# Kernel optimization log

Hardware: AMD Instinct MI355X
Metric: run time of the kernel (lower is better)

Reference implementation:

```python
import jax, jax.numpy as jnp
import numpy as np

B = 32; IMG = 224; P = 16; D = 768; NH = 12; HD = 64; L = 12; MLP = 3072; S0 = 197
NE = 10; LP = 40; NPL = 5; NC = 100; EPS = 1e-6
POS_PROMPT = (0, 1, 2, 3, 4)


def setup_inputs() -> dict:
    ks = jax.random.split(jax.random.key(0), 18)
    n = lambda k, shp: jax.random.normal(k, shp, jnp.float32) * 0.02
    return {
        "inputs": jax.random.normal(ks[0], (B, 3, IMG, IMG), jnp.float32),
        "expert_ids": jax.random.randint(ks[1], (B,), 0, NE),
        "patch_w": n(ks[2], (D, 3, P, P)),
        "patch_b": n(ks[3], (D,)),
        "cls_token": n(ks[4], (1, 1, D)),
        "pos_embed": n(ks[5], (1, S0, D)),
        "ln1_s": jnp.ones((L, D), jnp.float32),
        "ln1_b": jnp.zeros((L, D), jnp.float32),
        "qkv_w": n(ks[6], (L, D, 3 * D)),
        "qkv_b": n(ks[7], (L, 3 * D)),
        "proj_w": n(ks[8], (L, D, D)),
        "proj_b": n(ks[9], (L, D)),
        "ln2_s": jnp.ones((L, D), jnp.float32),
        "ln2_b": jnp.zeros((L, D), jnp.float32),
        "fc1_w": n(ks[10], (L, D, MLP)),
        "fc1_b": n(ks[11], (L, MLP)),
        "fc2_w": n(ks[12], (L, MLP, D)),
        "fc2_b": n(ks[13], (L, D)),
        "norm_s": jnp.ones((D,), jnp.float32),
        "norm_b": jnp.zeros((D,), jnp.float32),
        "prompts": jax.random.uniform(ks[14], (NPL, NE, LP, D), jnp.float32),
        "head_w": n(ks[15], (NE, D, NC)),
        "head_b": n(ks[16], (NE, NC)),
    }


def _ln(x, s, b):
    m = x.mean(-1, keepdims=True)
    v = ((x - m) ** 2).mean(-1, keepdims=True)
    return (x - m) * jax.lax.rsqrt(v + EPS) * s + b


def _forward(inputs, expert_ids, patch_w, patch_b, cls_token, pos_embed,
             ln1_s, ln1_b, qkv_w, qkv_b, proj_w, proj_b, ln2_s, ln2_b,
             fc1_w, fc1_b, fc2_w, fc2_b, norm_s, norm_b, prompts, head_w, head_b):
    # patch embed: conv stride 16 -> [B, D, 14, 14] -> [B, 196, D]
    x = jax.lax.conv_general_dilated(inputs, patch_w, (P, P), 'VALID',
                                     dimension_numbers=('NCHW', 'OIHW', 'NCHW'))
    x = x.reshape(B, D, -1).transpose(0, 2, 1) + patch_b
    x = jnp.concatenate([jnp.broadcast_to(cls_token, (B, 1, D)), x], axis=1) + pos_embed
    # per-sample expert prompt gather: [B, NPL, LP, D], plus cls pos bias
    bp = jnp.take(prompts, expert_ids, axis=1).transpose(1, 0, 2, 3) + pos_embed[0, 0]
    scale = 1.0 / np.sqrt(HD)
    for i in range(L):
        if i in POS_PROMPT:
            x = jnp.concatenate([x, bp[:, POS_PROMPT.index(i)]], axis=1)
        S = x.shape[1]
        h = _ln(x, ln1_s[i], ln1_b[i])
        qkv = (h @ qkv_w[i] + qkv_b[i]).reshape(B, S, 3, NH, HD).transpose(2, 0, 3, 1, 4)
        q, k, v = qkv[0], qkv[1], qkv[2]
        att = jax.nn.softmax(jnp.einsum('bhqd,bhkd->bhqk', q, k) * scale, axis=-1)
        o = jnp.einsum('bhqk,bhkd->bhqd', att, v).transpose(0, 2, 1, 3).reshape(B, S, D)
        x = x + o @ proj_w[i] + proj_b[i]
        h = _ln(x, ln2_s[i], ln2_b[i])
        x = x + jax.nn.gelu(h @ fc1_w[i] + fc1_b[i], approximate=False) @ fc2_w[i] + fc2_b[i]
        x = x[:, :S0]  # drop prompt tokens after each block
    feat = _ln(x, norm_s, norm_b)[:, 0]
    # per-sample expert head dispatch: gathered-weight batched matvec
    return jnp.einsum('bd,bdc->bc', feat, head_w[expert_ids]) + head_b[expert_ids]


def reference(inputs, expert_ids, patch_w, patch_b, cls_token, pos_embed,
              ln1_s, ln1_b, qkv_w, qkv_b, proj_w, proj_b, ln2_s, ln2_b,
              fc1_w, fc1_b, fc2_w, fc2_b, norm_s, norm_b, prompts, head_w, head_b):
    return _forward(inputs, expert_ids, patch_w, patch_b, cls_token, pos_embed,
                    ln1_s, ln1_b, qkv_w, qkv_b, proj_w, proj_b, ln2_s, ln2_b,
                    fc1_w, fc1_b, fc2_w, fc2_b, norm_s, norm_b, prompts, head_w, head_b)
```

## Files before the change

kernel.cpp:

```cpp
#include <hip/hip_runtime.h>

typedef unsigned short ushort_t;
typedef __attribute__((ext_vector_type(8))) short short8;
typedef __attribute__((ext_vector_type(4))) float floatx4;

#define D_    768
#define SMAX  237
#define S0_   197
#define RPAD  7680
#define NHEAD 12
#define BATCH 32


__device__ __forceinline__ ushort_t f2bf(float f) {
  union { float f; unsigned u; } v; v.f = f;
  unsigned r = v.u + 0x7FFFu + ((v.u >> 16) & 1u);
  return (ushort_t)(r >> 16);
}
__device__ __forceinline__ float bf2f(ushort_t u) {
  union { unsigned u; float f; } v; v.u = ((unsigned)u) << 16; return v.f;
}
__device__ __forceinline__ void async16(const void* g, void* l) {
  __builtin_amdgcn_global_load_lds((const __attribute__((address_space(1))) void*)g,
                                   (__attribute__((address_space(3))) void*)l, 16, 0, 0);
}

__global__ __launch_bounds__(256) void patchify_kernel(
    const float* __restrict__ in, ushort_t* __restrict__ Xp) {
  int rowid = blockIdx.x;
  int b = rowid / 196, p = rowid - b * 196;
  int py = p / 14, px = p - py * 14;
  int tid = threadIdx.x;
#pragma unroll
  for (int t = 0; t < 3; ++t) {
    int k = tid + t * 256;
    int c = k >> 8, rem = k & 255, i = rem >> 4, j = rem & 15;
    float v = in[(((size_t)b * 3 + c) * 224 + py * 16 + i) * 224 + px * 16 + j];
    Xp[(size_t)rowid * 768 + k] = f2bf(v);
  }
}

__global__ void cvt_bf16_kernel(const float* __restrict__ src, ushort_t* __restrict__ dst, int n) {
  int i = blockIdx.x * 256 + threadIdx.x;
  if (i < n) dst[i] = f2bf(src[i]);
}

__global__ void cls_fill_kernel(const float* __restrict__ cls, const float* __restrict__ pos,
                                float* __restrict__ X) {
  int b = blockIdx.x, d = threadIdx.x;
  X[(size_t)b * 768 + d] = cls[d] + pos[d];
}

__global__ void prompt_fill_kernel(const float* __restrict__ prompts, const float* __restrict__ pos,
                                   const int* __restrict__ eid, float* __restrict__ X, int layer) {
  int id = blockIdx.x;
  int b = id / 40, p = id - b * 40;
  int e = eid[b];
  float v = prompts[(((size_t)layer * 10 + e) * 40 + p) * 768 + threadIdx.x] + pos[threadIdx.x];
  X[((size_t)(197 + p) * 32 + b) * 768 + threadIdx.x] = v;
}

__global__ __launch_bounds__(256) void transpose_wts_kernel(
    const float* __restrict__ qkvw, const float* __restrict__ projw,
    const float* __restrict__ fc1w, const float* __restrict__ fc2w,
    ushort_t* __restrict__ wq, ushort_t* __restrict__ wp,
    ushort_t* __restrict__ w1, ushort_t* __restrict__ w2,
    int l0, int slot_mul) {
  int id = blockIdx.x;
  int l = l0 + id / 6912;
  int t = id % 6912;
  size_t s = (size_t)(l * slot_mul);
  const float* src; ushort_t* dst; int K, N;
  if (t < 1728)      { src = qkvw + (size_t)l * 768 * 2304; dst = wq + s * 2304 * 768; K = 768;  N = 2304; }
  else if (t < 2304) { src = projw + (size_t)l * 768 * 768;  dst = wp + s * 768 * 768;  K = 768;  N = 768;  t -= 1728; }
  else if (t < 4608) { src = fc1w + (size_t)l * 768 * 3072;  dst = w1 + s * 768 * 3072; K = 768;  N = 3072; t -= 2304; }
  else               { src = fc2w + (size_t)l * 3072 * 768;  dst = w2 + s * 3072 * 768; K = 3072; N = 768;  t -= 4608; }
  int ntn = N >> 5;
  int k0 = (t / ntn) * 32, n0 = (t % ntn) * 32;
  __shared__ float tile[32][33];
  int tx = threadIdx.x & 31, ty = threadIdx.x >> 5;
#pragma unroll
  for (int q = 0; q < 4; ++q) {
    int kk = q * 8 + ty;
    tile[kk][tx] = src[(size_t)(k0 + kk) * N + n0 + tx];
  }
  __syncthreads();
#pragma unroll
  for (int q = 0; q < 4; ++q) {
    int nn = q * 8 + ty;
    dst[(size_t)(n0 + nn) * K + k0 + tx] = f2bf(tile[tx][nn]);
  }
}

__global__ __launch_bounds__(256) void ln_kernel(
    const float* __restrict__ X, const float* __restrict__ s, const float* __restrict__ bt,
    ushort_t* __restrict__ H) {
  int row = blockIdx.x, tid = threadIdx.x;
  const float* xr = X + (size_t)row * 768;
  float v0 = xr[tid], v1 = xr[tid + 256], v2 = xr[tid + 512];
  float sum = v0 + v1 + v2;
  float sq = v0 * v0 + v1 * v1 + v2 * v2;
#pragma unroll
  for (int off = 32; off; off >>= 1) {
    sum += __shfl_down(sum, off, 64);
    sq  += __shfl_down(sq,  off, 64);
  }
  __shared__ float red[8];
  int wv = tid >> 6, ln = tid & 63;
  if (ln == 0) { red[wv] = sum; red[4 + wv] = sq; }
  __syncthreads();
  if (tid == 0) {
    red[0] = red[0] + red[1] + red[2] + red[3];
    red[4] = red[4] + red[5] + red[6] + red[7];
  }
  __syncthreads();
  float mean = red[0] * (1.f / 768.f);
  float var  = red[4] * (1.f / 768.f) - mean * mean;
  float rs = rsqrtf(var + 1e-6f);
  ushort_t* hr = H + (size_t)row * 768;
  hr[tid]       = f2bf((v0 - mean) * rs * s[tid]       + bt[tid]);
  hr[tid + 256] = f2bf((v1 - mean) * rs * s[tid + 256] + bt[tid + 256]);
  hr[tid + 512] = f2bf((v2 - mean) * rs * s[tid + 512] + bt[tid + 512]);
}

enum { EPI_BF16 = 0, EPI_GELU = 1, EPI_RESID = 2, EPI_PATCH = 3 };

template <int EPI>
__device__ __forceinline__ void epi_store(float accv, int row, int col,
                                          const float* bias, float* XO, ushort_t* O,
                                          const float* pos, int N) {
  if (EPI == EPI_BF16) {
    O[(size_t)row * N + col] = f2bf(accv + bias[col]);
  } else if (EPI == EPI_GELU) {
    float v = accv + bias[col];
    float g = 0.5f * v * (1.0f + erff(v * 0.70710678118f));
    O[(size_t)row * N + col] = f2bf(g);
  } else if (EPI == EPI_RESID) {
    XO[(size_t)row * 768 + col] += accv + bias[col];
  } else {
    int b = row / 196, p = row - b * 196;
    size_t orow = (size_t)(1 + p) * 32 + b;
    XO[orow * 768 + col] = accv + bias[col] + pos[(size_t)(1 + p) * 768 + col];
  }
}

template <int EPI>
__global__ __launch_bounds__(256) void gemm_kernel(
    const ushort_t* __restrict__ A, int lda,
    const ushort_t* __restrict__ BT,
    const float* __restrict__ bias,
    float* __restrict__ XO, ushort_t* __restrict__ O,
    const float* __restrict__ pos,
    int N, int K) {
  __shared__ ushort_t As[128 * 32];
  __shared__ ushort_t Bs[128 * 32];
  int m0 = blockIdx.y * 128, n0 = blockIdx.x * 128;
  int tid = threadIdx.x, lane = tid & 63, wv = tid >> 6;
  int wm = (wv >> 1) * 64, wn = (wv & 1) * 64;
  int fr = lane & 15, kg = lane >> 4;
  int sw = (kg ^ ((fr >> 1) & 3)) * 8;

  floatx4 acc[4][4];
#pragma unroll
  for (int i = 0; i < 4; ++i)
#pragma unroll
    for (int j = 0; j < 4; ++j) acc[i][j] = (floatx4){0.f, 0.f, 0.f, 0.f};

  for (int k0 = 0; k0 < K; k0 += 32) {
#pragma unroll
    for (int t = 0; t < 2; ++t) {
      int flat = (wv * 2 + t) * 64 + lane;
      int row = flat >> 2;
      int ch = ((flat & 3) ^ ((flat >> 3) & 3)) * 8;
      async16(A + (size_t)(m0 + row) * lda + k0 + ch, &As[(wv * 2 + t) * 512]);
      async16(BT + (size_t)(n0 + row) * K + k0 + ch, &Bs[(wv * 2 + t) * 512]);
    }
    __syncthreads();
    short8 af[4], bfr[4];
#pragma unroll
    for (int i = 0; i < 4; ++i) af[i] = *(const short8*)&As[(wm + i * 16 + fr) * 32 + sw];
#pragma unroll
    for (int j = 0; j < 4; ++j) bfr[j] = *(const short8*)&Bs[(wn + j * 16 + fr) * 32 + sw];
#pragma unroll
    for (int i = 0; i < 4; ++i)
#pragma unroll
      for (int j = 0; j < 4; ++j)
        acc[i][j] = __builtin_amdgcn_mfma_f32_16x16x32_bf16(af[i], bfr[j], acc[i][j], 0, 0, 0);
    __syncthreads();
  }

  int rbase = (lane >> 4) * 4;
#pragma unroll
  for (int i = 0; i < 4; ++i)
#pragma unroll
    for (int j = 0; j < 4; ++j) {
      int col = n0 + wn + j * 16 + fr;
#pragma unroll
      for (int r = 0; r < 4; ++r)
        epi_store<EPI>(acc[i][j][r], m0 + wm + i * 16 + rbase + r, col, bias, XO, O, pos, N);
    }
}

template <int EPI>
__global__ __launch_bounds__(256) void gemm64_kernel(
    const ushort_t* __restrict__ A, int lda,
    const ushort_t* __restrict__ BT,
    const float* __restrict__ bias,
    float* __restrict__ XO, ushort_t* __restrict__ O,
    const float* __restrict__ pos,
    int N, int K) {
  __shared__ ushort_t As[64 * 32];
  __shared__ ushort_t Bs[128 * 32];
  int m0 = blockIdx.y * 64, n0 = blockIdx.x * 128;
  int tid = threadIdx.x, lane = tid & 63, wv = tid >> 6;
  int wm = (wv >> 1) * 32, wn = (wv & 1) * 64;
  int fr = lane & 15, kg = lane >> 4;
  int sw = (kg ^ ((fr >> 1) & 3)) * 8;

  floatx4 acc[2][4];
#pragma unroll
  for (int i = 0; i < 2; ++i)
#pragma unroll
    for (int j = 0; j < 4; ++j) acc[i][j] = (floatx4){0.f, 0.f, 0.f, 0.f};

  for (int k0 = 0; k0 < K; k0 += 32) {
    {
      int flat = wv * 64 + lane;
      int row = flat >> 2;
      int ch = ((flat & 3) ^ ((flat >> 3) & 3)) * 8;
      async16(A + (size_t)(m0 + row) * lda + k0 + ch, &As[wv * 512]);
    }
#pragma unroll
    for (int t = 0; t < 2; ++t) {
      int flat = (wv * 2 + t) * 64 + lane;
      int row = flat >> 2;
      int ch = ((flat & 3) ^ ((flat >> 3) & 3)) * 8;
      async16(BT + (size_t)(n0 + row) * K + k0 + ch, &Bs[(wv * 2 + t) * 512]);
    }
    __syncthreads();
    short8 af[2], bfr[4];
#pragma unroll
    for (int i = 0; i < 2; ++i) af[i] = *(const short8*)&As[(wm + i * 16 + fr) * 32 + sw];
#pragma unroll
    for (int j = 0; j < 4; ++j) bfr[j] = *(const short8*)&Bs[(wn + j * 16 + fr) * 32 + sw];
#pragma unroll
    for (int i = 0; i < 2; ++i)
#pragma unroll
      for (int j = 0; j < 4; ++j)
        acc[i][j] = __builtin_amdgcn_mfma_f32_16x16x32_bf16(af[i], bfr[j], acc[i][j], 0, 0, 0);
    __syncthreads();
  }

  int rbase = (lane >> 4) * 4;
#pragma unroll
  for (int i = 0; i < 2; ++i)
#pragma unroll
    for (int j = 0; j < 4; ++j) {
      int col = n0 + wn + j * 16 + fr;
#pragma unroll
      for (int r = 0; r < 4; ++r)
        epi_store<EPI>(acc[i][j][r], m0 + wm + i * 16 + rbase + r, col, bias, XO, O, pos, N);
    }
}

__global__ __launch_bounds__(256) void attn_kernel(ushort_t* __restrict__ qkv, int S) {
  __shared__ ushort_t Kc[64 * 64];
  __shared__ ushort_t Vt[64 * 72];
  __shared__ ushort_t Pb[4][16 * 72];
  int id = blockIdx.x;
  int qc = id & 3, bh = id >> 2;
  int b = bh / NHEAD, h = bh - b * NHEAD;
  int tid = threadIdx.x, lane = tid & 63, wv = tid >> 6;
  int fr = lane & 15, kg = lane >> 4;
  int q0 = qc * 64 + wv * 16;

  int qr = q0 + fr; if (qr > S - 1) qr = S - 1;
  const ushort_t* qp = qkv + ((size_t)qr * 32 + b) * 2304 + h * 64 + kg * 8;
  short8 qf0 = *(const short8*)qp;
  short8 qf1 = *(const short8*)(qp + 32);

  floatx4 oacc[4];
#pragma unroll
  for (int j = 0; j < 4; ++j) oacc[j] = (floatx4){0.f, 0.f, 0.f, 0.f};
  float lsum[4] = {0.f, 0.f, 0.f, 0.f};

  int ksw = kg ^ (fr & 7);
  int kst_g = (lane & 7) ^ ((lane >> 3) & 7);

  for (int c = 0; c < 4; ++c) {
    int key0 = c * 64;
    __syncthreads();
#pragma unroll
    for (int t = 0; t < 2; ++t) {
      int f = (wv * 2 + t) * 64 + lane;
      int kr = key0 + (f >> 3); if (kr > S - 1) kr = S - 1;
      async16(qkv + ((size_t)kr * 32 + b) * 2304 + 768 + h * 64 + kst_g * 8,
              &Kc[(wv * 2 + t) * 512]);
    }
#pragma unroll
    for (int t = 0; t < 2; ++t) {
      int kc = wv * 2 + t;
      int vr = key0 + lane; if (vr > S - 1) vr = S - 1;
      short8 vv = *(const short8*)(qkv + ((size_t)vr * 32 + b) * 2304 + 1536 + h * 64 + kc * 8);
#pragma unroll
      for (int e = 0; e < 8; ++e) Vt[(kc * 8 + e) * 72 + lane] = (ushort_t)vv[e];
    }
    __syncthreads();

    floatx4 sacc[4];
#pragma unroll
    for (int j = 0; j < 4; ++j) sacc[j] = (floatx4){0.f, 0.f, 0.f, 0.f};
#pragma unroll
    for (int j = 0; j < 4; ++j) {
      int krow = j * 16 + fr;
      short8 b0 = *(const short8*)&Kc[krow * 64 + ksw * 8];
      short8 b1 = *(const short8*)&Kc[krow * 64 + (ksw ^ 4) * 8];
      sacc[j] = __builtin_amdgcn_mfma_f32_16x16x32_bf16(qf0, b0, sacc[j], 0, 0, 0);
      sacc[j] = __builtin_amdgcn_mfma_f32_16x16x32_bf16(qf1, b1, sacc[j], 0, 0, 0);
    }

#pragma unroll
    for (int j = 0; j < 4; ++j) {
      int key = key0 + j * 16 + fr;
      bool valid = key < S;
#pragma unroll
      for (int r = 0; r < 4; ++r) {
        float e = valid ? __expf(sacc[j][r] * 0.125f) : 0.f;
        lsum[r] += e;
        Pb[wv][(kg * 4 + r) * 72 + j * 16 + fr] = f2bf(e);
      }
    }
    __syncthreads();

    const ushort_t* pp = &Pb[wv][fr * 72 + kg * 8];
    short8 p0 = *(const short8*)pp;
    short8 p1 = *(const short8*)(pp + 32);
#pragma unroll
    for (int j = 0; j < 4; ++j) {
      const ushort_t* vp = &Vt[(j * 16 + fr) * 72 + kg * 8];
      short8 v0 = *(const short8*)vp;
      short8 v1 = *(const short8*)(vp + 32);
      oacc[j] = __builtin_amdgcn_mfma_f32_16x16x32_bf16(p0, v0, oacc[j], 0, 0, 0);
      oacc[j] = __builtin_amdgcn_mfma_f32_16x16x32_bf16(p1, v1, oacc[j], 0, 0, 0);
    }
  }

#pragma unroll
  for (int r = 0; r < 4; ++r) {
#pragma unroll
    for (int m = 1; m <= 8; m <<= 1) lsum[r] += __shfl_xor(lsum[r], m, 64);
  }
#pragma unroll
  for (int r = 0; r < 4; ++r) {
    int q = q0 + kg * 4 + r;
    if (q < S) {
      float inv = 1.f / lsum[r];
      ushort_t* op = qkv + ((size_t)q * 32 + b) * 2304 + h * 64;
#pragma unroll
      for (int j = 0; j < 4; ++j) op[j * 16 + fr] = f2bf(oacc[j][r] * inv);
    }
  }
}

__global__ __launch_bounds__(256) void head_kernel(
    const float* __restrict__ X, const float* __restrict__ ns, const float* __restrict__ nb,
    const int* __restrict__ eid, const float* __restrict__ hw, const float* __restrict__ hb,
    float* __restrict__ out) {
  int b = blockIdx.x, tid = threadIdx.x;
  const float* xr = X + (size_t)b * 768;
  float v0 = xr[tid], v1 = xr[tid + 256], v2 = xr[tid + 512];
  float sum = v0 + v1 + v2;
  float sq = v0 * v0 + v1 * v1 + v2 * v2;
#pragma unroll
  for (int off = 32; off; off >>= 1) {
    sum += __shfl_down(sum, off, 64);
    sq  += __shfl_down(sq,  off, 64);
  }
  __shared__ float red[8];
  __shared__ float feat[768];
  int wv = tid >> 6, ln = tid & 63;
  if (ln == 0) { red[wv] = sum; red[4 + wv] = sq; }
  __syncthreads();
  if (tid == 0) {
    red[0] = red[0] + red[1] + red[2] + red[3];
    red[4] = red[4] + red[5] + red[6] + red[7];
  }
  __syncthreads();
  float mean = red[0] * (1.f / 768.f);
  float var  = red[4] * (1.f / 768.f) - mean * mean;
  float rs = rsqrtf(var + 1e-6f);
  feat[tid]       = (v0 - mean) * rs * ns[tid]       + nb[tid];
  feat[tid + 256] = (v1 - mean) * rs * ns[tid + 256] + nb[tid + 256];
  feat[tid + 512] = (v2 - mean) * rs * ns[tid + 512] + nb[tid + 512];
  __syncthreads();
  int e = eid[b];
  if (tid < 100) {
    float a = hb[e * 100 + tid];
    const float* w = hw + (size_t)e * 768 * 100 + tid;
#pragma unroll 4
    for (int d = 0; d < 768; ++d) a += feat[d] * w[(size_t)d * 100];
    out[b * 100 + tid] = a;
  }
}

extern "C" void kernel_launch(void* const* d_in, const int* in_sizes, int n_in,
                              void* d_out, int out_size, void* d_ws, size_t ws_size,
                              hipStream_t stream) {
  const float* inputs     = (const float*)d_in[0];
  const int*   expert_ids = (const int*)d_in[1];
  const float* patch_w    = (const float*)d_in[2];
  const float* patch_b    = (const float*)d_in[3];
  const float* cls_token  = (const float*)d_in[4];
  const float* pos_embed  = (const float*)d_in[5];
  const float* ln1_s      = (const float*)d_in[6];
  const float* ln1_b      = (const float*)d_in[7];
  const float* qkv_w      = (const float*)d_in[8];
  const float* qkv_b      = (const float*)d_in[9];
  const float* proj_w     = (const float*)d_in[10];
  const float* proj_b     = (const float*)d_in[11];
  const float* ln2_s      = (const float*)d_in[12];
  const float* ln2_b      = (const float*)d_in[13];
  const float* fc1_w      = (const float*)d_in[14];
  const float* fc1_b      = (const float*)d_in[15];
  const float* fc2_w      = (const float*)d_in[16];
  const float* fc2_b      = (const float*)d_in[17];
  const float* norm_s     = (const float*)d_in[18];
  const float* norm_b     = (const float*)d_in[19];
  const float* prompts    = (const float*)d_in[20];
  const float* head_w     = (const float*)d_in[21];
  const float* head_b     = (const float*)d_in[22];
  float* out = (float*)d_out;

  const size_t kHoistNeed = 289100000ull;
  bool hoist = ws_size >= kHoistNeed;
  size_t slots = hoist ? 12 : 1;

  char* ws = (char*)d_ws;
  size_t off = 0;
  ushort_t* WTp = (ushort_t*)(ws + off); off += (size_t)768 * 768 * 2;
  ushort_t* WQ  = (ushort_t*)(ws + off); off += slots * 2304 * 768 * 2;
  ushort_t* WP  = (ushort_t*)(ws + off); off += slots * 768 * 768 * 2;
  ushort_t* W1  = (ushort_t*)(ws + off); off += slots * 768 * 3072 * 2;
  ushort_t* W2  = (ushort_t*)(ws + off); off += slots * 3072 * 768 * 2;
  float*    X   = (float*)(ws + off);    off += (size_t)RPAD * 768 * 4;
  ushort_t* H   = (ushort_t*)(ws + off); off += (size_t)RPAD * 768 * 2;
  ushort_t* QKV = (ushort_t*)(ws + off); off += (size_t)RPAD * 2304 * 2;
  ushort_t* MID = (ushort_t*)(ws + off); off += (size_t)RPAD * 3072 * 2;
  ushort_t* XP  = MID;

  cvt_bf16_kernel<<<(768 * 768 + 255) / 256, 256, 0, stream>>>(patch_w, WTp, 768 * 768);
  patchify_kernel<<<6272, 256, 0, stream>>>(inputs, XP);
  gemm64_kernel<EPI_PATCH><<<dim3(6, 98), 256, 0, stream>>>(
      XP, 768, WTp, patch_b, X, nullptr, pos_embed, 768, 768);
  cls_fill_kernel<<<BATCH, 768, 0, stream>>>(cls_token, pos_embed, X);

  if (hoist)
    transpose_wts_kernel<<<6912 * 12, 256, 0, stream>>>(
        qkv_w, proj_w, fc1_w, fc2_w, WQ, WP, W1, W2, 0, 1);

  for (int i = 0; i < 12; ++i) {
    int S = (i < 5) ? SMAX : S0_;
    int MT = (i < 5) ? 60 : 50;
    if (i < 5)
      prompt_fill_kernel<<<BATCH * 40, 768, 0, stream>>>(prompts, pos_embed, expert_ids, X, i);
    if (!hoist)
      transpose_wts_kernel<<<6912, 256, 0, stream>>>(
          qkv_w, proj_w, fc1_w, fc2_w, WQ, WP, W1, W2, i, 0);
    ushort_t* WQi = WQ + (hoist ? (size_t)i * 2304 * 768 : 0);
    ushort_t* WPi = WP + (hoist ? (size_t)i * 768 * 768 : 0);
    ushort_t* W1i = W1 + (hoist ? (size_t)i * 768 * 3072 : 0);
    ushort_t* W2i = W2 + (hoist ? (size_t)i * 3072 * 768 : 0);

    ln_kernel<<<MT * 128, 256, 0, stream>>>(X, ln1_s + i * 768, ln1_b + i * 768, H);
    gemm_kernel<EPI_BF16><<<dim3(18, MT), 256, 0, stream>>>(
        H, 768, WQi, qkv_b + i * 2304, nullptr, QKV, nullptr, 2304, 768);
    attn_kernel<<<BATCH * NHEAD * 4, 256, 0, stream>>>(QKV, S);
    gemm64_kernel<EPI_RESID><<<dim3(6, MT * 2), 256, 0, stream>>>(
        QKV, 2304, WPi, proj_b + i * 768, X, nullptr, nullptr, 768, 768);
    ln_kernel<<<MT * 128, 256, 0, stream>>>(X, ln2_s + i * 768, ln2_b + i * 768, H);
    gemm_kernel<EPI_GELU><<<dim3(24, MT), 256, 0, stream>>>(
        H, 768, W1i, fc1_b + i * 3072, nullptr, MID, nullptr, 3072, 768);
    gemm64_kernel<EPI_RESID><<<dim3(6, MT * 2), 256, 0, stream>>>(
        MID, 3072, W2i, fc2_b + i * 768, X, nullptr, nullptr, 768, 3072);
  }

  head_kernel<<<BATCH, 256, 0, stream>>>(X, norm_s, norm_b, expert_ids, head_w, head_b, out);
}
```

Before: 3.508 ms.

## Deepen GEMM K-tile to 64, vectorize LN and weight transpose, retile residual GEMMs

The GEMM kernels now stage 64-wide K slices in LDS with an 8-way XOR swizzle and run two MFMA sub-steps per barrier pair, halving the number of synchronisations per K. Layernorm processes one row per wavefront with vector loads and shuffle-only reductions, which removes the shared-memory barriers. The weight transpose uses 64x64 tiles with vector loads and 16-byte bf16 stores. The proj and fc2 residual GEMMs switch from 64-row to 128-row tiles, trading fewer blocks for more reuse.

```diff
diff --git a/kernel.cpp b/kernel.cpp
--- a/kernel.cpp
+++ b/kernel.cpp
@@ -2,6 +2,7 @@
 
 typedef unsigned short ushort_t;
 typedef __attribute__((ext_vector_type(8))) short short8;
+typedef __attribute__((ext_vector_type(4))) short shortx4;
 typedef __attribute__((ext_vector_type(4))) float floatx4;
 
 #define D_    768
@@ -67,60 +68,72 @@
     ushort_t* __restrict__ w1, ushort_t* __restrict__ w2,
     int l0, int slot_mul) {
   int id = blockIdx.x;
-  int l = l0 + id / 6912;
-  int t = id % 6912;
+  int l = l0 + id / 1728;
+  int t = id % 1728;
   size_t s = (size_t)(l * slot_mul);
   const float* src; ushort_t* dst; int K, N;
-  if (t < 1728)      { src = qkvw + (size_t)l * 768 * 2304; dst = wq + s * 2304 * 768; K = 768;  N = 2304; }
-  else if (t < 2304) { src = projw + (size_t)l * 768 * 768;  dst = wp + s * 768 * 768;  K = 768;  N = 768;  t -= 1728; }
-  else if (t < 4608) { src = fc1w + (size_t)l * 768 * 3072;  dst = w1 + s * 768 * 3072; K = 768;  N = 3072; t -= 2304; }
-  else               { src = fc2w + (size_t)l * 3072 * 768;  dst = w2 + s * 3072 * 768; K = 3072; N = 768;  t -= 4608; }
-  int ntn = N >> 5;
-  int k0 = (t / ntn) * 32, n0 = (t % ntn) * 32;
-  __shared__ float tile[32][33];
-  int tx = threadIdx.x & 31, ty = threadIdx.x >> 5;
+  if (t < 432)       { src = qkvw + (size_t)l * 768 * 2304; dst = wq + s * 2304 * 768; K = 768;  N = 2304; }
+  else if (t < 576)  { src = projw + (size_t)l * 768 * 768;  dst = wp + s * 768 * 768;  K = 768;  N = 768;  t -= 432; }
+  else if (t < 1152) { src = fc1w + (size_t)l * 768 * 3072;  dst = w1 + s * 768 * 3072; K = 768;  N = 3072; t -= 576; }
+  else               { src = fc2w + (size_t)l * 3072 * 768;  dst = w2 + s * 3072 * 768; K = 3072; N = 768;  t -= 1152; }
+  int ntn = N >> 6;
+  int k0 = (t / ntn) * 64, n0 = (t % ntn) * 64;
+  __shared__ float tile[64][65];
+  int tid = threadIdx.x;
 #pragma unroll
   for (int q = 0; q < 4; ++q) {
-    int kk = q * 8 + ty;
-    tile[kk][tx] = src[(size_t)(k0 + kk) * N + n0 + tx];
+    int slot = q * 256 + tid;
+    int r = slot >> 4, c4 = (slot & 15) * 4;
+    floatx4 v = *(const floatx4*)&src[(size_t)(k0 + r) * N + n0 + c4];
+    tile[r][c4] = v[0]; tile[r][c4 + 1] = v[1]; tile[r][c4 + 2] = v[2]; tile[r][c4 + 3] = v[3];
   }
   __syncthreads();
 #pragma unroll
-  for (int q = 0; q < 4; ++q) {
-    int nn = q * 8 + ty;
-    dst[(size_t)(n0 + nn) * K + k0 + tx] = f2bf(tile[tx][nn]);
+  for (int q = 0; q < 2; ++q) {
+    int slot = q * 256 + tid;
+    int n = slot >> 3, kc = (slot & 7) * 8;
+    short8 o;
+#pragma unroll
+    for (int e = 0; e < 8; ++e) o[e] = (short)f2bf(tile[kc + e][n]);
+    *(short8*)&dst[(size_t)(n0 + n) * K + k0 + kc] = o;
   }
 }
 
 __global__ __launch_bounds__(256) void ln_kernel(
     const float* __restrict__ X, const float* __restrict__ s, const float* __restrict__ bt,
     ushort_t* __restrict__ H) {
-  int row = blockIdx.x, tid = threadIdx.x;
+  int row = blockIdx.x * 4 + (threadIdx.x >> 6);
+  int lane = threadIdx.x & 63;
   const float* xr = X + (size_t)row * 768;
-  float v0 = xr[tid], v1 = xr[tid + 256], v2 = xr[tid + 512];
-  float sum = v0 + v1 + v2;
-  float sq = v0 * v0 + v1 * v1 + v2 * v2;
-#pragma unroll
-  for (int off = 32; off; off >>= 1) {
-    sum += __shfl_down(sum, off, 64);
-    sq  += __shfl_down(sq,  off, 64);
-  }
-  __shared__ float red[8];
-  int wv = tid >> 6, ln = tid & 63;
-  if (ln == 0) { red[wv] = sum; red[4 + wv] = sq; }
-  __syncthreads();
-  if (tid == 0) {
-    red[0] = red[0] + red[1] + red[2] + red[3];
-    red[4] = red[4] + red[5] + red[6] + red[7];
-  }
-  __syncthreads();
-  float mean = red[0] * (1.f / 768.f);
-  float var  = red[4] * (1.f / 768.f) - mean * mean;
+  floatx4 v0 = *(const floatx4*)&xr[lane * 4];
+  floatx4 v1 = *(const floatx4*)&xr[256 + lane * 4];
+  floatx4 v2 = *(const floatx4*)&xr[512 + lane * 4];
+  float sum = 0.f, sq = 0.f;
+#pragma unroll
+  for (int e = 0; e < 4; ++e) {
+    sum += v0[e] + v1[e] + v2[e];
+    sq  += v0[e] * v0[e] + v1[e] * v1[e] + v2[e] * v2[e];
+  }
+#pragma unroll
+  for (int m = 1; m <= 32; m <<= 1) {
+    sum += __shfl_xor(sum, m, 64);
+    sq  += __shfl_xor(sq,  m, 64);
+  }
+  float mean = sum * (1.f / 768.f);
+  float var  = sq * (1.f / 768.f) - mean * mean;
   float rs = rsqrtf(var + 1e-6f);
   ushort_t* hr = H + (size_t)row * 768;
-  hr[tid]       = f2bf((v0 - mean) * rs * s[tid]       + bt[tid]);
-  hr[tid + 256] = f2bf((v1 - mean) * rs * s[tid + 256] + bt[tid + 256]);
-  hr[tid + 512] = f2bf((v2 - mean) * rs * s[tid + 512] + bt[tid + 512]);
+#pragma unroll
+  for (int w = 0; w < 3; ++w) {
+    const floatx4 v = (w == 0) ? v0 : (w == 1) ? v1 : v2;
+    shortx4 o;
+#pragma unroll
+    for (int e = 0; e < 4; ++e) {
+      int d = w * 256 + lane * 4 + e;
+      o[e] = (short)f2bf((v[e] - mean) * rs * s[d] + bt[d]);
+    }
+    *(shortx4*)&hr[w * 256 + lane * 4] = o;
+  }
 }
 
 enum { EPI_BF16 = 0, EPI_GELU = 1, EPI_RESID = 2, EPI_PATCH = 3 };
@@ -152,13 +165,13 @@
     float* __restrict__ XO, ushort_t* __restrict__ O,
     const float* __restrict__ pos,
     int N, int K) {
-  __shared__ ushort_t As[128 * 32];
-  __shared__ ushort_t Bs[128 * 32];
+  __shared__ ushort_t As[128 * 64];
+  __shared__ ushort_t Bs[128 * 64];
   int m0 = blockIdx.y * 128, n0 = blockIdx.x * 128;
   int tid = threadIdx.x, lane = tid & 63, wv = tid >> 6;
   int wm = (wv >> 1) * 64, wn = (wv & 1) * 64;
   int fr = lane & 15, kg = lane >> 4;
-  int sw = (kg ^ ((fr >> 1) & 3)) * 8;
+  int sw = (fr >> 1) & 7;
 
   floatx4 acc[4][4];
 #pragma unroll
@@ -166,26 +179,31 @@
 #pragma unroll
     for (int j = 0; j < 4; ++j) acc[i][j] = (floatx4){0.f, 0.f, 0.f, 0.f};
 
-  for (int k0 = 0; k0 < K; k0 += 32) {
-#pragma unroll
-    for (int t = 0; t < 2; ++t) {
-      int flat = (wv * 2 + t) * 64 + lane;
-      int row = flat >> 2;
-      int ch = ((flat & 3) ^ ((flat >> 3) & 3)) * 8;
-      async16(A + (size_t)(m0 + row) * lda + k0 + ch, &As[(wv * 2 + t) * 512]);
-      async16(BT + (size_t)(n0 + row) * K + k0 + ch, &Bs[(wv * 2 + t) * 512]);
-    }
-    __syncthreads();
-    short8 af[4], bfr[4];
-#pragma unroll
-    for (int i = 0; i < 4; ++i) af[i] = *(const short8*)&As[(wm + i * 16 + fr) * 32 + sw];
-#pragma unroll
-    for (int j = 0; j < 4; ++j) bfr[j] = *(const short8*)&Bs[(wn + j * 16 + fr) * 32 + sw];
-#pragma unroll
-    for (int i = 0; i < 4; ++i)
+  for (int k0 = 0; k0 < K; k0 += 64) {
+#pragma unroll
+    for (int t = 0; t < 4; ++t) {
+      int flat = (wv * 4 + t) * 64 + lane;
+      int row = flat >> 3;
+      int ch = ((flat & 7) ^ ((row >> 1) & 7)) * 8;
+      async16(A + (size_t)(m0 + row) * lda + k0 + ch, &As[(wv * 4 + t) * 512]);
+      async16(BT + (size_t)(n0 + row) * K + k0 + ch, &Bs[(wv * 4 + t) * 512]);
+    }
+    __syncthreads();
+#pragma unroll
+    for (int kh = 0; kh < 2; ++kh) {
+      short8 af[4], bfr[4];
+#pragma unroll
+      for (int i = 0; i < 4; ++i)
+        af[i] = *(const short8*)&As[(wm + i * 16 + fr) * 64 + (((kh * 4 + kg) ^ sw) * 8)];
 #pragma unroll
       for (int j = 0; j < 4; ++j)
-        acc[i][j] = __builtin_amdgcn_mfma_f32_16x16x32_bf16(af[i], bfr[j], acc[i][j], 0, 0, 0);
+        bfr[j] = *(const short8*)&Bs[(wn + j * 16 + fr) * 64 + (((kh * 4 + kg) ^ sw) * 8)];
+#pragma unroll
+      for (int i = 0; i < 4; ++i)
+#pragma unroll
+        for (int j = 0; j < 4; ++j)
+          acc[i][j] = __builtin_amdgcn_mfma_f32_16x16x32_bf16(af[i], bfr[j], acc[i][j], 0, 0, 0);
+    }
     __syncthreads();
   }
 
@@ -209,13 +227,13 @@
     float* __restrict__ XO, ushort_t* __restrict__ O,
     const float* __restrict__ pos,
     int N, int K) {
-  __shared__ ushort_t As[64 * 32];
-  __shared__ ushort_t Bs[128 * 32];
+  __shared__ ushort_t As[64 * 64];
+  __shared__ ushort_t Bs[128 * 64];
   int m0 = blockIdx.y * 64, n0 = blockIdx.x * 128;
   int tid = threadIdx.x, lane = tid & 63, wv = tid >> 6;
   int wm = (wv >> 1) * 32, wn = (wv & 1) * 64;
   int fr = lane & 15, kg = lane >> 4;
-  int sw = (kg ^ ((fr >> 1) & 3)) * 8;
+  int sw = (fr >> 1) & 7;
 
   floatx4 acc[2][4];
 #pragma unroll
@@ -223,31 +241,37 @@
 #pragma unroll
     for (int j = 0; j < 4; ++j) acc[i][j] = (floatx4){0.f, 0.f, 0.f, 0.f};
 
-  for (int k0 = 0; k0 < K; k0 += 32) {
-    {
-      int flat = wv * 64 + lane;
-      int row = flat >> 2;
-      int ch = ((flat & 3) ^ ((flat >> 3) & 3)) * 8;
-      async16(A + (size_t)(m0 + row) * lda + k0 + ch, &As[wv * 512]);
-    }
+  for (int k0 = 0; k0 < K; k0 += 64) {
 #pragma unroll
     for (int t = 0; t < 2; ++t) {
       int flat = (wv * 2 + t) * 64 + lane;
-      int row = flat >> 2;
-      int ch = ((flat & 3) ^ ((flat >> 3) & 3)) * 8;
-      async16(BT + (size_t)(n0 + row) * K + k0 + ch, &Bs[(wv * 2 + t) * 512]);
-    }
-    __syncthreads();
-    short8 af[2], bfr[4];
-#pragma unroll
-    for (int i = 0; i < 2; ++i) af[i] = *(const short8*)&As[(wm + i * 16 + fr) * 32 + sw];
-#pragma unroll
-    for (int j = 0; j < 4; ++j) bfr[j] = *(const short8*)&Bs[(wn + j * 16 + fr) * 32 + sw];
-#pragma unroll
-    for (int i = 0; i < 2; ++i)
+      int row = flat >> 3;
+      int ch = ((flat & 7) ^ ((row >> 1) & 7)) * 8;
+      async16(A + (size_t)(m0 + row) * lda + k0 + ch, &As[(wv * 2 + t) * 512]);
+    }
+#pragma unroll
+    for (int t = 0; t < 4; ++t) {
+      int flat = (wv * 4 + t) * 64 + lane;
+      int row = flat >> 3;
+      int ch = ((flat & 7) ^ ((row >> 1) & 7)) * 8;
+      async16(BT + (size_t)(n0 + row) * K + k0 + ch, &Bs[(wv * 4 + t) * 512]);
+    }
+    __syncthreads();
+#pragma unroll
+    for (int kh = 0; kh < 2; ++kh) {
+      short8 af[2], bfr[4];
+#pragma unroll
+      for (int i = 0; i < 2; ++i)
+        af[i] = *(const short8*)&As[(wm + i * 16 + fr) * 64 + (((kh * 4 + kg) ^ sw) * 8)];
 #pragma unroll
       for (int j = 0; j < 4; ++j)
-        acc[i][j] = __builtin_amdgcn_mfma_f32_16x16x32_bf16(af[i], bfr[j], acc[i][j], 0, 0, 0);
+        bfr[j] = *(const short8*)&Bs[(wn + j * 16 + fr) * 64 + (((kh * 4 + kg) ^ sw) * 8)];
+#pragma unroll
+      for (int i = 0; i < 2; ++i)
+#pragma unroll
+        for (int j = 0; j < 4; ++j)
+          acc[i][j] = __builtin_amdgcn_mfma_f32_16x16x32_bf16(af[i], bfr[j], acc[i][j], 0, 0, 0);
+    }
     __syncthreads();
   }
 
@@ -455,7 +479,7 @@
   cls_fill_kernel<<<BATCH, 768, 0, stream>>>(cls_token, pos_embed, X);
 
   if (hoist)
-    transpose_wts_kernel<<<6912 * 12, 256, 0, stream>>>(
+    transpose_wts_kernel<<<1728 * 12, 256, 0, stream>>>(
         qkv_w, proj_w, fc1_w, fc2_w, WQ, WP, W1, W2, 0, 1);
 
   for (int i = 0; i < 12; ++i) {
@@ -464,23 +488,23 @@
     if (i < 5)
       prompt_fill_kernel<<<BATCH * 40, 768, 0, stream>>>(prompts, pos_embed, expert_ids, X, i);
     if (!hoist)
-      transpose_wts_kernel<<<6912, 256, 0, stream>>>(
+      transpose_wts_kernel<<<1728, 256, 0, stream>>>(
           qkv_w, proj_w, fc1_w, fc2_w, WQ, WP, W1, W2, i, 0);
     ushort_t* WQi = WQ + (hoist ? (size_t)i * 2304 * 768 : 0);
     ushort_t* WPi = WP + (hoist ? (size_t)i * 768 * 768 : 0);
     ushort_t* W1i = W1 + (hoist ? (size_t)i * 768 * 3072 : 0);
     ushort_t* W2i = W2 + (hoist ? (size_t)i * 3072 * 768 : 0);
 
-    ln_kernel<<<MT * 128, 256, 0, stream>>>(X, ln1_s + i * 768, ln1_b + i * 768, H);
+    ln_kernel<<<MT * 32, 256, 0, stream>>>(X, ln1_s + i * 768, ln1_b + i * 768, H);
     gemm_kernel<EPI_BF16><<<dim3(18, MT), 256, 0, stream>>>(
         H, 768, WQi, qkv_b + i * 2304, nullptr, QKV, nullptr, 2304, 768);
     attn_kernel<<<BATCH * NHEAD * 4, 256, 0, stream>>>(QKV, S);
-    gemm64_kernel<EPI_RESID><<<dim3(6, MT * 2), 256, 0, stream>>>(
+    gemm_kernel<EPI_RESID><<<dim3(6, MT), 256, 0, stream>>>(
         QKV, 2304, WPi, proj_b + i * 768, X, nullptr, nullptr, 768, 768);
-    ln_kernel<<<MT * 128, 256, 0, stream>>>(X, ln2_s + i * 768, ln2_b + i * 768, H);
+    ln_kernel<<<MT * 32, 256, 0, stream>>>(X, ln2_s + i * 768, ln2_b + i * 768, H);
     gemm_kernel<EPI_GELU><<<dim3(24, MT), 256, 0, stream>>>(
         H, 768, W1i, fc1_b + i * 3072, nullptr, MID, nullptr, 3072, 768);
-    gemm64_kernel<EPI_RESID><<<dim3(6, MT * 2), 256, 0, stream>>>(
+    gemm_kernel<EPI_RESID><<<dim3(6, MT), 256, 0, stream>>>(
         MID, 3072, W2i, fc2_b + i * 768, X, nullptr, nullptr, 768, 3072);
   }
 
```

Result: faster. 3.390 ms (-3.3%).
